# Kernel tuning notes

Measured on AMD Instinct MI355X. Metric: run time of the kernel, lower is better.

The kernel has to match this reference:

```python
import jax, jax.numpy as jnp
import numpy as np

NUM_HEADS = 4
EMBED = 128
QKV = 128
OUT = 128
HEAD_DIM = QKV // NUM_HEADS  # 32
BATCH = 16384
SEQ = 16


def setup_inputs() -> dict:
    key = jax.random.key(0)
    k_x, k_q, k_k, k_v, k_o = jax.random.split(key, 5)
    x = jax.random.normal(k_x, (BATCH, SEQ, EMBED), dtype=jnp.float32)
    w_q = jax.random.normal(k_q, (NUM_HEADS, EMBED, HEAD_DIM), dtype=jnp.float32)
    w_k = jax.random.normal(k_k, (NUM_HEADS, EMBED, HEAD_DIM), dtype=jnp.float32)
    w_v = jax.random.normal(k_v, (NUM_HEADS, EMBED, HEAD_DIM), dtype=jnp.float32)
    w_o = jax.random.normal(k_o, (NUM_HEADS, HEAD_DIM, OUT), dtype=jnp.float32)
    return {"x": x, "w_q": w_q, "w_k": w_k, "w_v": w_v, "w_o": w_o}


def reference(x, w_q, w_k, w_v, w_o) -> jnp.ndarray:
    # x: [B, S, E]; w_q/k/v: [H, E, D]; w_o: [H, D, O]
    head_dim = w_q.shape[-1]
    scale = jnp.asarray(head_dim, x.dtype) ** -0.5
    Q = jnp.einsum("bse,hed->bhsd", x, w_q)
    K = jnp.einsum("bse,hed->bhsd", x, w_k)
    V = jnp.einsum("bse,hed->bhsd", x, w_v)
    scores = jnp.einsum("bhsd,bhtd->bhst", Q * scale, K)  # [B, H, S, S]
    A = jax.nn.softmax(scores, axis=-1)
    H = jnp.einsum("bhst,bhtd->bhsd", A, V)
    # per-head output projection summed over heads
    out = jnp.einsum("bhsd,hdo->bso", H, w_o)
    return out
```

## Files before the change

kernel.cpp:

```cpp
#include <hip/hip_runtime.h>

#define BATCHES 16384
#define BPW     32
#define NWG     (BATCHES / BPW)

typedef __attribute__((ext_vector_type(8))) _Float16 h8;
typedef __attribute__((ext_vector_type(4))) float f4;

#define MFMA16(a, b, c) __builtin_amdgcn_mfma_f32_16x16x32_f16((a), (b), (c), 0, 0, 0)

__device__ __forceinline__ h8 h8_zero() {
  h8 v;
#pragma unroll
  for (int j = 0; j < 8; ++j) v[j] = (_Float16)0.0f;
  return v;
}

__global__ __launch_bounds__(256, 1)
void attn16(const float* __restrict__ xg,
            const float* __restrict__ wq,
            const float* __restrict__ wk,
            const float* __restrict__ wv,
            const float* __restrict__ wo,
            float* __restrict__ outg)
{
  __shared__ __align__(16) _Float16 s_xh[2][2048];
  __shared__ __align__(16) _Float16 s_xl[2][2048];
  __shared__ __align__(16) float    s_qk[4][1024];
  __shared__ __align__(16) _Float16 s_vt[4][512];
  __shared__ __align__(16) _Float16 s_a [4][256];
  __shared__ __align__(16) _Float16 s_h [2048];

  const int tid  = threadIdx.x;
  const int wid  = tid >> 6;
  const int lane = tid & 63;
  const int lhi  = lane >> 4;
  const int llo  = lane & 15;

  h8 wqh[4][2], wql[4][2], wkh[4][2], wkl[4][2], wvf[4][2], wof[4][2];
#pragma unroll
  for (int ks = 0; ks < 4; ++ks) {
#pragma unroll
    for (int nt = 0; nt < 2; ++nt) {
#pragma unroll
      for (int j = 0; j < 8; ++j) {
        const int e = ks * 32 + lhi * 8 + j;
        const int d = nt * 16 + llo;
        const float q = wq[(size_t)wid * 4096 + e * 32 + d];
        const float k = wk[(size_t)wid * 4096 + e * 32 + d];
        const float v = wv[(size_t)wid * 4096 + e * 32 + d];
        const _Float16 qh = (_Float16)q;
        const _Float16 kh = (_Float16)k;
        wqh[ks][nt][j] = qh;
        wql[ks][nt][j] = (_Float16)(q - (float)qh);
        wkh[ks][nt][j] = kh;
        wkl[ks][nt][j] = (_Float16)(k - (float)kh);
        wvf[ks][nt][j] = (_Float16)v;
        const int o = wid * 32 + nt * 16 + llo;
        wof[ks][nt][j] = (_Float16)wo[(size_t)ks * 4096 + (lhi * 8 + j) * 128 + o];
      }
    }
  }

  const int b0 = blockIdx.x * BPW;
  const float scale = 0.17677669529663687f;

  {
    const float4* src = (const float4*)(xg + (size_t)b0 * 2048);
    const float4 a = src[tid * 2 + 0];
    const float4 b = src[tid * 2 + 1];
    const int m  = tid >> 4;
    const int sl = (tid & 15) ^ (m & 7);
    const float f[8] = {a.x, a.y, a.z, a.w, b.x, b.y, b.z, b.w};
    h8 hi, lo;
#pragma unroll
    for (int j = 0; j < 8; ++j) {
      const _Float16 h = (_Float16)f[j];
      hi[j] = h;
      lo[j] = (_Float16)(f[j] - (float)h);
    }
    *(h8*)&s_xh[0][m * 128 + sl * 8] = hi;
    *(h8*)&s_xl[0][m * 128 + sl * 8] = lo;
  }
  __syncthreads();

  int cur = 0;
  for (int bi = 0; bi < BPW; ++bi) {
    const int b = b0 + bi;

    float4 pa = {}, pb = {};
    const bool hasNext = (bi + 1 < BPW);
    if (hasNext) {
      const float4* src = (const float4*)(xg + (size_t)(b + 1) * 2048);
      pa = src[tid * 2 + 0];
      pb = src[tid * 2 + 1];
    }

    f4 qacc[2] = {{0,0,0,0},{0,0,0,0}};
    f4 kacc[2] = {{0,0,0,0},{0,0,0,0}};
    f4 vacc[2] = {{0,0,0,0},{0,0,0,0}};
#pragma unroll
    for (int ks = 0; ks < 4; ++ks) {
      const int sl = (ks * 4 + lhi) ^ (llo & 7);
      const h8 ah = *(const h8*)&s_xh[cur][llo * 128 + sl * 8];
      const h8 al = *(const h8*)&s_xl[cur][llo * 128 + sl * 8];
#pragma unroll
      for (int nt = 0; nt < 2; ++nt) {
        qacc[nt] = MFMA16(ah, wqh[ks][nt], qacc[nt]);
        qacc[nt] = MFMA16(ah, wql[ks][nt], qacc[nt]);
        qacc[nt] = MFMA16(al, wqh[ks][nt], qacc[nt]);
        kacc[nt] = MFMA16(ah, wkh[ks][nt], kacc[nt]);
        kacc[nt] = MFMA16(ah, wkl[ks][nt], kacc[nt]);
        kacc[nt] = MFMA16(al, wkh[ks][nt], kacc[nt]);
        vacc[nt] = MFMA16(ah, wvf[ks][nt], vacc[nt]);
      }
    }

    float* qb = s_qk[wid];
#pragma unroll
    for (int nt = 0; nt < 2; ++nt) {
#pragma unroll
      for (int r = 0; r < 4; ++r) {
        const int t = lhi * 4 + r;
        const int d = nt * 16 + llo;
        const int sl = (d >> 2) ^ (t & 7);
        qb[t * 32 + sl * 4 + (d & 3)]       = qacc[nt][r];
        qb[512 + t * 32 + sl * 4 + (d & 3)] = kacc[nt][r];
        s_vt[wid][d * 16 + t] = (_Float16)vacc[nt][r];
      }
    }

    h8 qhf, qlf, khf, klf;
    {
      const int s0 = (lhi * 2 + 0) ^ (llo & 7);
      const int s1 = (lhi * 2 + 1) ^ (llo & 7);
      const f4 qa = *(const f4*)&qb[llo * 32 + s0 * 4];
      const f4 qc = *(const f4*)&qb[llo * 32 + s1 * 4];
      const f4 ka = *(const f4*)&qb[512 + llo * 32 + s0 * 4];
      const f4 kc = *(const f4*)&qb[512 + llo * 32 + s1 * 4];
#pragma unroll
      for (int j = 0; j < 4; ++j) {
        _Float16 h;
        h = (_Float16)qa[j]; qhf[j]     = h; qlf[j]     = (_Float16)(qa[j] - (float)h);
        h = (_Float16)qc[j]; qhf[4 + j] = h; qlf[4 + j] = (_Float16)(qc[j] - (float)h);
        h = (_Float16)ka[j]; khf[j]     = h; klf[j]     = (_Float16)(ka[j] - (float)h);
        h = (_Float16)kc[j]; khf[4 + j] = h; klf[4 + j] = (_Float16)(kc[j] - (float)h);
      }
    }
    f4 sacc = {0,0,0,0};
    sacc = MFMA16(qhf, khf, sacc);
    sacc = MFMA16(qhf, klf, sacc);
    sacc = MFMA16(qlf, khf, sacc);

#pragma unroll
    for (int r = 0; r < 4; ++r) {
      const float v = sacc[r] * scale;
      float mx = v;
      mx = fmaxf(mx, __shfl_xor(mx, 1));
      mx = fmaxf(mx, __shfl_xor(mx, 2));
      mx = fmaxf(mx, __shfl_xor(mx, 4));
      mx = fmaxf(mx, __shfl_xor(mx, 8));
      const float p = __expf(v - mx);
      float sm = p;
      sm += __shfl_xor(sm, 1);
      sm += __shfl_xor(sm, 2);
      sm += __shfl_xor(sm, 4);
      sm += __shfl_xor(sm, 8);
      const float a = p * __builtin_amdgcn_rcpf(sm);
      const int t = lhi * 4 + r;
      s_a[wid][t * 16 + llo] = (_Float16)a;
    }

    h8 af = h8_zero(), v0f = h8_zero(), v1f = h8_zero();
    if (lhi < 2) {
      af  = *(const h8*)&s_a[wid][llo * 16 + lhi * 8];
      v0f = *(const h8*)&s_vt[wid][(0  + llo) * 16 + lhi * 8];
      v1f = *(const h8*)&s_vt[wid][(16 + llo) * 16 + lhi * 8];
    }
    f4 hacc0 = {0,0,0,0}, hacc1 = {0,0,0,0};
    hacc0 = MFMA16(af, v0f, hacc0);
    hacc1 = MFMA16(af, v1f, hacc1);

#pragma unroll
    for (int nt2 = 0; nt2 < 2; ++nt2) {
      const f4 hv = nt2 ? hacc1 : hacc0;
#pragma unroll
      for (int r = 0; r < 4; ++r) {
        const int t = lhi * 4 + r;
        const int d = wid * 32 + nt2 * 16 + llo;
        const int sl = (d >> 3) ^ (t & 7);
        s_h[t * 128 + sl * 8 + (d & 7)] = (_Float16)hv[r];
      }
    }
    __syncthreads();

    f4 oacc0 = {0,0,0,0}, oacc1 = {0,0,0,0};
#pragma unroll
    for (int ks = 0; ks < 4; ++ks) {
      const int sl = (ks * 4 + lhi) ^ (llo & 7);
      const h8 hf = *(const h8*)&s_h[llo * 128 + sl * 8];
      oacc0 = MFMA16(hf, wof[ks][0], oacc0);
      oacc1 = MFMA16(hf, wof[ks][1], oacc1);
    }
    float* ob = outg + (size_t)b * 2048;
#pragma unroll
    for (int r = 0; r < 4; ++r) {
      const int t = lhi * 4 + r;
      ob[t * 128 + wid * 32 + llo]      = oacc0[r];
      ob[t * 128 + wid * 32 + 16 + llo] = oacc1[r];
    }

    if (hasNext) {
      const int m  = tid >> 4;
      const int sl = (tid & 15) ^ (m & 7);
      const float f[8] = {pa.x, pa.y, pa.z, pa.w, pb.x, pb.y, pb.z, pb.w};
      h8 hi, lo;
#pragma unroll
      for (int j = 0; j < 8; ++j) {
        const _Float16 h = (_Float16)f[j];
        hi[j] = h;
        lo[j] = (_Float16)(f[j] - (float)h);
      }
      *(h8*)&s_xh[cur ^ 1][m * 128 + sl * 8] = hi;
      *(h8*)&s_xl[cur ^ 1][m * 128 + sl * 8] = lo;
    }
    __syncthreads();
    cur ^= 1;
  }
}

extern "C" void kernel_launch(void* const* d_in, const int* in_sizes, int n_in,
                              void* d_out, int out_size, void* d_ws, size_t ws_size,
                              hipStream_t stream) {
  const float* x  = (const float*)d_in[0];
  const float* wq = (const float*)d_in[1];
  const float* wk = (const float*)d_in[2];
  const float* wv = (const float*)d_in[3];
  const float* wo = (const float*)d_in[4];
  float* out = (float*)d_out;
  attn16<<<NWG, 256, 0, stream>>>(x, wq, wk, wv, wo, out);
}
```

Before: 343.9 us.

## Compute transposed Q/K/V tiles to keep attention in registers, drop LDS round-trips

```diff
diff --git a/kernel.cpp b/kernel.cpp
--- a/kernel.cpp
+++ b/kernel.cpp
@@ -1,20 +1,16 @@
 #include <hip/hip_runtime.h>
 
 #define BATCHES 16384
-#define BPW     32
+#define BPW     8
 #define NWG     (BATCHES / BPW)
 
 typedef __attribute__((ext_vector_type(8))) _Float16 h8;
+typedef __attribute__((ext_vector_type(4))) _Float16 h4;
 typedef __attribute__((ext_vector_type(4))) float f4;
 
-#define MFMA16(a, b, c) __builtin_amdgcn_mfma_f32_16x16x32_f16((a), (b), (c), 0, 0, 0)
-
-__device__ __forceinline__ h8 h8_zero() {
-  h8 v;
-#pragma unroll
-  for (int j = 0; j < 8; ++j) v[j] = (_Float16)0.0f;
-  return v;
-}
+#define MFMA32(a, b, c) __builtin_amdgcn_mfma_f32_16x16x32_f16((a), (b), (c), 0, 0, 0)
+#define MFMA16(a, b, c) __builtin_amdgcn_mfma_f32_16x16x16f16((a), (b), (c), 0, 0, 0)
+
 
 __global__ __launch_bounds__(256, 1)
 void attn16(const float* __restrict__ xg,
@@ -26,10 +22,7 @@
 {
   __shared__ __align__(16) _Float16 s_xh[2][2048];
   __shared__ __align__(16) _Float16 s_xl[2][2048];
-  __shared__ __align__(16) float    s_qk[4][1024];
-  __shared__ __align__(16) _Float16 s_vt[4][512];
-  __shared__ __align__(16) _Float16 s_a [4][256];
-  __shared__ __align__(16) _Float16 s_h [2048];
+  __shared__ __align__(16) _Float16 s_ht[2][2048];
 
   const int tid  = threadIdx.x;
   const int wid  = tid >> 6;
@@ -37,33 +30,45 @@
   const int lhi  = lane >> 4;
   const int llo  = lane & 15;
 
-  h8 wqh[4][2], wql[4][2], wkh[4][2], wkl[4][2], wvf[4][2], wof[4][2];
+  const float scale = 0.17677669529663687f;
+
+  h8 wqh[4][2], wql[4][2], wkh[4][2], wkl[4][2], wvf[4][2];
 #pragma unroll
   for (int ks = 0; ks < 4; ++ks) {
 #pragma unroll
-    for (int nt = 0; nt < 2; ++nt) {
+    for (int mt = 0; mt < 2; ++mt) {
 #pragma unroll
       for (int j = 0; j < 8; ++j) {
         const int e = ks * 32 + lhi * 8 + j;
-        const int d = nt * 16 + llo;
-        const float q = wq[(size_t)wid * 4096 + e * 32 + d];
+        const int d = mt * 16 + llo;
+        const float q = wq[(size_t)wid * 4096 + e * 32 + d] * scale;
         const float k = wk[(size_t)wid * 4096 + e * 32 + d];
         const float v = wv[(size_t)wid * 4096 + e * 32 + d];
         const _Float16 qh = (_Float16)q;
         const _Float16 kh = (_Float16)k;
-        wqh[ks][nt][j] = qh;
-        wql[ks][nt][j] = (_Float16)(q - (float)qh);
-        wkh[ks][nt][j] = kh;
-        wkl[ks][nt][j] = (_Float16)(k - (float)kh);
-        wvf[ks][nt][j] = (_Float16)v;
-        const int o = wid * 32 + nt * 16 + llo;
-        wof[ks][nt][j] = (_Float16)wo[(size_t)ks * 4096 + (lhi * 8 + j) * 128 + o];
+        wqh[ks][mt][j] = qh;
+        wql[ks][mt][j] = (_Float16)(q - (float)qh);
+        wkh[ks][mt][j] = kh;
+        wkl[ks][mt][j] = (_Float16)(k - (float)kh);
+        wvf[ks][mt][j] = (_Float16)v;
+      }
+    }
+  }
+  h4 wof[8][2];
+#pragma unroll
+  for (int ks = 0; ks < 8; ++ks) {
+#pragma unroll
+    for (int mt = 0; mt < 2; ++mt) {
+#pragma unroll
+      for (int j = 0; j < 4; ++j) {
+        const int hd = ks * 16 + lhi * 4 + j;
+        const int o  = (wid * 2 + mt) * 16 + llo;
+        wof[ks][mt][j] = (_Float16)wo[(size_t)(hd >> 5) * 4096 + (hd & 31) * 128 + o];
       }
     }
   }
 
   const int b0 = blockIdx.x * BPW;
-  const float scale = 0.17677669529663687f;
 
   {
     const float4* src = (const float4*)(xg + (size_t)b0 * 2048);
@@ -85,131 +90,93 @@
   __syncthreads();
 
   int cur = 0;
+#pragma unroll 1
   for (int bi = 0; bi < BPW; ++bi) {
     const int b = b0 + bi;
+    const bool hasNext = (bi + 1 < BPW);
 
     float4 pa = {}, pb = {};
-    const bool hasNext = (bi + 1 < BPW);
     if (hasNext) {
       const float4* src = (const float4*)(xg + (size_t)(b + 1) * 2048);
       pa = src[tid * 2 + 0];
       pb = src[tid * 2 + 1];
     }
 
-    f4 qacc[2] = {{0,0,0,0},{0,0,0,0}};
-    f4 kacc[2] = {{0,0,0,0},{0,0,0,0}};
-    f4 vacc[2] = {{0,0,0,0},{0,0,0,0}};
+    h8 xh[4], xl[4];
 #pragma unroll
     for (int ks = 0; ks < 4; ++ks) {
       const int sl = (ks * 4 + lhi) ^ (llo & 7);
-      const h8 ah = *(const h8*)&s_xh[cur][llo * 128 + sl * 8];
-      const h8 al = *(const h8*)&s_xl[cur][llo * 128 + sl * 8];
-#pragma unroll
-      for (int nt = 0; nt < 2; ++nt) {
-        qacc[nt] = MFMA16(ah, wqh[ks][nt], qacc[nt]);
-        qacc[nt] = MFMA16(ah, wql[ks][nt], qacc[nt]);
-        qacc[nt] = MFMA16(al, wqh[ks][nt], qacc[nt]);
-        kacc[nt] = MFMA16(ah, wkh[ks][nt], kacc[nt]);
-        kacc[nt] = MFMA16(ah, wkl[ks][nt], kacc[nt]);
-        kacc[nt] = MFMA16(al, wkh[ks][nt], kacc[nt]);
-        vacc[nt] = MFMA16(ah, wvf[ks][nt], vacc[nt]);
-      }
-    }
-
-    float* qb = s_qk[wid];
-#pragma unroll
-    for (int nt = 0; nt < 2; ++nt) {
-#pragma unroll
-      for (int r = 0; r < 4; ++r) {
-        const int t = lhi * 4 + r;
-        const int d = nt * 16 + llo;
-        const int sl = (d >> 2) ^ (t & 7);
-        qb[t * 32 + sl * 4 + (d & 3)]       = qacc[nt][r];
-        qb[512 + t * 32 + sl * 4 + (d & 3)] = kacc[nt][r];
-        s_vt[wid][d * 16 + t] = (_Float16)vacc[nt][r];
-      }
-    }
-
-    h8 qhf, qlf, khf, klf;
-    {
-      const int s0 = (lhi * 2 + 0) ^ (llo & 7);
-      const int s1 = (lhi * 2 + 1) ^ (llo & 7);
-      const f4 qa = *(const f4*)&qb[llo * 32 + s0 * 4];
-      const f4 qc = *(const f4*)&qb[llo * 32 + s1 * 4];
-      const f4 ka = *(const f4*)&qb[512 + llo * 32 + s0 * 4];
-      const f4 kc = *(const f4*)&qb[512 + llo * 32 + s1 * 4];
+      xh[ks] = *(const h8*)&s_xh[cur][llo * 128 + sl * 8];
+      xl[ks] = *(const h8*)&s_xl[cur][llo * 128 + sl * 8];
+    }
+
+    f4 qt[2] = {{0,0,0,0},{0,0,0,0}};
+    f4 kt[2] = {{0,0,0,0},{0,0,0,0}};
+    f4 vv[2] = {{0,0,0,0},{0,0,0,0}};
+#pragma unroll
+    for (int ks = 0; ks < 4; ++ks) {
+#pragma unroll
+      for (int mt = 0; mt < 2; ++mt) {
+        qt[mt] = MFMA32(wqh[ks][mt], xh[ks], qt[mt]);
+        qt[mt] = MFMA32(wql[ks][mt], xh[ks], qt[mt]);
+        qt[mt] = MFMA32(wqh[ks][mt], xl[ks], qt[mt]);
+        kt[mt] = MFMA32(wkh[ks][mt], xh[ks], kt[mt]);
+        kt[mt] = MFMA32(wkl[ks][mt], xh[ks], kt[mt]);
+        kt[mt] = MFMA32(wkh[ks][mt], xl[ks], kt[mt]);
+        vv[mt] = MFMA32(xh[ks], wvf[ks][mt], vv[mt]);
+      }
+    }
+
+    h4 qth[2], qtl[2], kth[2], ktl[2], vh[2];
+#pragma unroll
+    for (int mt = 0; mt < 2; ++mt) {
 #pragma unroll
       for (int j = 0; j < 4; ++j) {
         _Float16 h;
-        h = (_Float16)qa[j]; qhf[j]     = h; qlf[j]     = (_Float16)(qa[j] - (float)h);
-        h = (_Float16)qc[j]; qhf[4 + j] = h; qlf[4 + j] = (_Float16)(qc[j] - (float)h);
-        h = (_Float16)ka[j]; khf[j]     = h; klf[j]     = (_Float16)(ka[j] - (float)h);
-        h = (_Float16)kc[j]; khf[4 + j] = h; klf[4 + j] = (_Float16)(kc[j] - (float)h);
-      }
-    }
-    f4 sacc = {0,0,0,0};
-    sacc = MFMA16(qhf, khf, sacc);
-    sacc = MFMA16(qhf, klf, sacc);
-    sacc = MFMA16(qlf, khf, sacc);
-
-#pragma unroll
-    for (int r = 0; r < 4; ++r) {
-      const float v = sacc[r] * scale;
-      float mx = v;
-      mx = fmaxf(mx, __shfl_xor(mx, 1));
-      mx = fmaxf(mx, __shfl_xor(mx, 2));
-      mx = fmaxf(mx, __shfl_xor(mx, 4));
-      mx = fmaxf(mx, __shfl_xor(mx, 8));
-      const float p = __expf(v - mx);
-      float sm = p;
-      sm += __shfl_xor(sm, 1);
-      sm += __shfl_xor(sm, 2);
-      sm += __shfl_xor(sm, 4);
-      sm += __shfl_xor(sm, 8);
-      const float a = p * __builtin_amdgcn_rcpf(sm);
-      const int t = lhi * 4 + r;
-      s_a[wid][t * 16 + llo] = (_Float16)a;
-    }
-
-    h8 af = h8_zero(), v0f = h8_zero(), v1f = h8_zero();
-    if (lhi < 2) {
-      af  = *(const h8*)&s_a[wid][llo * 16 + lhi * 8];
-      v0f = *(const h8*)&s_vt[wid][(0  + llo) * 16 + lhi * 8];
-      v1f = *(const h8*)&s_vt[wid][(16 + llo) * 16 + lhi * 8];
-    }
-    f4 hacc0 = {0,0,0,0}, hacc1 = {0,0,0,0};
-    hacc0 = MFMA16(af, v0f, hacc0);
-    hacc1 = MFMA16(af, v1f, hacc1);
-
-#pragma unroll
-    for (int nt2 = 0; nt2 < 2; ++nt2) {
-      const f4 hv = nt2 ? hacc1 : hacc0;
-#pragma unroll
-      for (int r = 0; r < 4; ++r) {
-        const int t = lhi * 4 + r;
-        const int d = wid * 32 + nt2 * 16 + llo;
-        const int sl = (d >> 3) ^ (t & 7);
-        s_h[t * 128 + sl * 8 + (d & 7)] = (_Float16)hv[r];
-      }
-    }
-    __syncthreads();
-
-    f4 oacc0 = {0,0,0,0}, oacc1 = {0,0,0,0};
-#pragma unroll
-    for (int ks = 0; ks < 4; ++ks) {
-      const int sl = (ks * 4 + lhi) ^ (llo & 7);
-      const h8 hf = *(const h8*)&s_h[llo * 128 + sl * 8];
-      oacc0 = MFMA16(hf, wof[ks][0], oacc0);
-      oacc1 = MFMA16(hf, wof[ks][1], oacc1);
-    }
-    float* ob = outg + (size_t)b * 2048;
-#pragma unroll
-    for (int r = 0; r < 4; ++r) {
-      const int t = lhi * 4 + r;
-      ob[t * 128 + wid * 32 + llo]      = oacc0[r];
-      ob[t * 128 + wid * 32 + 16 + llo] = oacc1[r];
-    }
-
+        h = (_Float16)qt[mt][j]; qth[mt][j] = h; qtl[mt][j] = (_Float16)(qt[mt][j] - (float)h);
+        h = (_Float16)kt[mt][j]; kth[mt][j] = h; ktl[mt][j] = (_Float16)(kt[mt][j] - (float)h);
+        vh[mt][j] = (_Float16)vv[mt][j];
+      }
+    }
+
+    f4 st = {0,0,0,0};
+#pragma unroll
+    for (int ks2 = 0; ks2 < 2; ++ks2) {
+      st = MFMA16(kth[ks2], qth[ks2], st);
+      st = MFMA16(ktl[ks2], qth[ks2], st);
+      st = MFMA16(kth[ks2], qtl[ks2], st);
+    }
+
+    float mx = fmaxf(fmaxf(st[0], st[1]), fmaxf(st[2], st[3]));
+    mx = fmaxf(mx, __shfl_xor(mx, 16));
+    mx = fmaxf(mx, __shfl_xor(mx, 32));
+    const float p0 = __expf(st[0] - mx);
+    const float p1 = __expf(st[1] - mx);
+    const float p2 = __expf(st[2] - mx);
+    const float p3 = __expf(st[3] - mx);
+    float sm = p0 + p1 + p2 + p3;
+    sm += __shfl_xor(sm, 16);
+    sm += __shfl_xor(sm, 32);
+    const float rinv = __builtin_amdgcn_rcpf(sm);
+    h4 an;
+    an[0] = (_Float16)(p0 * rinv);
+    an[1] = (_Float16)(p1 * rinv);
+    an[2] = (_Float16)(p2 * rinv);
+    an[3] = (_Float16)(p3 * rinv);
+
+    f4 ht0 = {0,0,0,0}, ht1 = {0,0,0,0};
+    ht0 = MFMA16(vh[0], an, ht0);
+    ht1 = MFMA16(vh[1], an, ht1);
+
+#pragma unroll
+    for (int mt = 0; mt < 2; ++mt) {
+      const f4 hv = mt ? ht1 : ht0;
+      h4 hh;
+#pragma unroll
+      for (int j = 0; j < 4; ++j) hh[j] = (_Float16)hv[j];
+      const int u = (wid * 8 + mt * 4 + lhi) ^ ((llo & 7) << 2);
+      *(h4*)&s_ht[cur][llo * 128 + u * 4] = hh;
+    }
     if (hasNext) {
       const int m  = tid >> 4;
       const int sl = (tid & 15) ^ (m & 7);
@@ -225,6 +192,19 @@
       *(h8*)&s_xl[cur ^ 1][m * 128 + sl * 8] = lo;
     }
     __syncthreads();
+
+    f4 oa0 = {0,0,0,0}, oa1 = {0,0,0,0};
+#pragma unroll
+    for (int ks = 0; ks < 8; ++ks) {
+      const int u = (ks * 4 + lhi) ^ ((llo & 7) << 2);
+      const h4 hf = *(const h4*)&s_ht[cur][llo * 128 + u * 4];
+      oa0 = MFMA16(wof[ks][0], hf, oa0);
+      oa1 = MFMA16(wof[ks][1], hf, oa1);
+    }
+    float* ob = outg + (size_t)b * 2048 + llo * 128 + wid * 32 + lhi * 4;
+    *(float4*)&ob[0]  = *(const float4*)&oa0;
+    *(float4*)&ob[16] = *(const float4*)&oa1;
+
     cur ^= 1;
   }
 }
```

After: 293.5 us. 1.17x faster.
